# Performance work log

Hardware: AMD Instinct MI355X
Metric: run time of the kernel (lower is better)

Reference implementation:

```python
import jax, jax.numpy as jnp
import numpy as np

N_NODES = 50000
N_EDGES = 800000
NUM_FEATURES = 128
H1, H2, H3 = 256, 512, 256


def setup_inputs() -> dict:
    key = jax.random.key(0)
    ks = jax.random.split(key, 14)

    def lin(kw, fan_in, fan_out):
        # torch nn.Linear-style init, stored as [in, out] for x @ W
        bound = 1.0 / np.sqrt(fan_in)
        W = jax.random.uniform(kw, (fan_in, fan_out), jnp.float32, -bound, bound)
        b = jnp.zeros((fan_out,), jnp.float32)
        return W, b

    x = jax.random.normal(ks[0], (N_NODES, NUM_FEATURES), jnp.float32)
    edge_index = jax.random.randint(ks[1], (2, N_EDGES), 0, N_NODES, jnp.int64 if jax.config.jax_enable_x64 else jnp.int32)

    W1, b1 = lin(ks[2], NUM_FEATURES, H1)
    W2, b2 = lin(ks[3], H1, H2)
    W3, b3 = lin(ks[4], H2, H3)
    Wf1, bf1 = lin(ks[5], H3, 128)
    Wf2, bf2 = lin(ks[6], 128, 64)
    Wf3, bf3 = lin(ks[7], 64, 1)

    return {"x": x, "edge_index": edge_index,
            "W1": W1, "b1": b1, "W2": W2, "b2": b2, "W3": W3, "b3": b3,
            "Wf1": Wf1, "bf1": bf1, "Wf2": Wf2, "bf2": bf2, "Wf3": Wf3, "bf3": bf3}


def gcn_conv(x, W, b, row, col, dinv_row_col, n):
    # PyG GCNConv: out = D^{-1/2} (A+I) D^{-1/2} (x W) + b, self-loops already in row/col
    h = x @ W                              # [N, out]
    msg = h[row] * dinv_row_col[:, None]   # gather + edge-wise scale: [E+N, out]
    return jax.ops.segment_sum(msg, col, num_segments=n) + b


def reference(x, edge_index, W1, b1, W2, b2, W3, b3, Wf1, bf1, Wf2, bf2, Wf3, bf3):
    n = x.shape[0]
    loop = jnp.arange(n, dtype=edge_index.dtype)
    row = jnp.concatenate([edge_index[0], loop])   # sources (with self-loops)
    col = jnp.concatenate([edge_index[1], loop])   # targets (with self-loops)

    # symmetric normalization (computed once; identical for all three convs)
    deg = jax.ops.segment_sum(jnp.ones(col.shape[0], x.dtype), col, num_segments=n)
    dinv = jnp.where(deg > 0, jax.lax.rsqrt(deg), 0.0)
    norm = dinv[row] * dinv[col]                   # [E+N]

    h = jax.nn.relu(gcn_conv(x, W1, b1, row, col, norm, n))
    h = jax.nn.relu(gcn_conv(h, W2, b2, row, col, norm, n))
    h = jax.nn.relu(gcn_conv(h, W3, b3, row, col, norm, n))

    g = jnp.mean(h, axis=0, keepdims=True)         # [1, H3]
    g = jax.nn.relu(g @ Wf1 + bf1)
    g = jax.nn.relu(g @ Wf2 + bf2)
    return g @ Wf3 + bf3                           # [1, 1]
```

## Files before the change

kernel.cpp:

```cpp
#include <hip/hip_runtime.h>
#include <hip/hip_bf16.h>

#define N_NODES 50000
#define N_EDGES 800000
#define N_BUCKETS 64
#define M_PAD 50048
#define SCAN_NB 196

typedef short short8 __attribute__((ext_vector_type(8)));
typedef float floatx4 __attribute__((ext_vector_type(4)));

__device__ __forceinline__ unsigned short f2bf(float f) {
    unsigned u = __float_as_uint(f);
    unsigned r = (u + 0x7fff + ((u >> 16) & 1)) >> 16;
    return (unsigned short)r;
}
__device__ __forceinline__ float bf2f(unsigned short h) {
    return __uint_as_float(((unsigned)h) << 16);
}
__device__ __forceinline__ void expand2(unsigned u, float& lo, float& hi) {
    lo = __uint_as_float(u << 16);
    hi = __uint_as_float(u & 0xffff0000u);
}
__device__ __forceinline__ void accum8(float* a, uint4 g, float w) {
    float lo, hi;
    expand2(g.x, lo, hi); a[0] += lo * w; a[1] += hi * w;
    expand2(g.y, lo, hi); a[2] += lo * w; a[3] += hi * w;
    expand2(g.z, lo, hi); a[4] += lo * w; a[5] += hi * w;
    expand2(g.w, lo, hi); a[6] += lo * w; a[7] += hi * w;
}

__device__ __forceinline__ void gload16(const void* gp, void* lp) {
    __builtin_amdgcn_global_load_lds(
        (const __attribute__((address_space(1))) unsigned int*)gp,
        (__attribute__((address_space(3))) unsigned int*)lp,
        16, 0, 0);
}

__global__ void k_init(int* __restrict__ cnt, float* __restrict__ gb) {
    int i = blockIdx.x * blockDim.x + threadIdx.x;
    if (i < N_NODES) cnt[i] = 0;
    if (i < N_BUCKETS * 256) gb[i] = 0.0f;
}

__global__ void k_count(const int* __restrict__ col, int* __restrict__ cnt) {
    int e = blockIdx.x * blockDim.x + threadIdx.x;
    if (e < N_EDGES) atomicAdd(&cnt[col[e]], 1);
}

__global__ __launch_bounds__(256) void k_scanA(const int* __restrict__ cnt,
                                               int* __restrict__ bsum) {
    __shared__ int red[256];
    int t = threadIdx.x;
    int i = blockIdx.x * 256 + t;
    red[t] = (i < N_NODES) ? cnt[i] : 0;
    __syncthreads();
    for (int d = 128; d > 0; d >>= 1) {
        if (t < d) red[t] += red[t + d];
        __syncthreads();
    }
    if (t == 0) bsum[blockIdx.x] = red[0];
}

__global__ __launch_bounds__(256) void k_scanB(const int* __restrict__ bsum,
                                               int* __restrict__ bbase,
                                               int* __restrict__ off) {
    __shared__ int sc[256];
    int t = threadIdx.x;
    sc[t] = (t < SCAN_NB) ? bsum[t] : 0;
    __syncthreads();
    for (int d = 1; d < 256; d <<= 1) {
        int v = 0;
        if (t >= d) v = sc[t - d];
        __syncthreads();
        if (t >= d) sc[t] += v;
        __syncthreads();
    }
    if (t < SCAN_NB) bbase[t] = sc[t] - bsum[t];
    if (t == 0) off[N_NODES] = N_EDGES + N_NODES;
    if (t == 0) off[N_NODES] = N_EDGES;
}

__global__ __launch_bounds__(256) void k_scanC(const int* __restrict__ cnt,
                                               const int* __restrict__ bbase,
                                               int* __restrict__ off,
                                               int* __restrict__ cursor,
                                               float* __restrict__ dinv) {
    __shared__ int sc[256];
    int t = threadIdx.x;
    int i = blockIdx.x * 256 + t;
    int c = (i < N_NODES) ? cnt[i] : 0;
    sc[t] = c;
    __syncthreads();
    for (int d = 1; d < 256; d <<= 1) {
        int v = 0;
        if (t >= d) v = sc[t - d];
        __syncthreads();
        if (t >= d) sc[t] += v;
        __syncthreads();
    }
    if (i < N_NODES) {
        int excl = sc[t] - c + bbase[blockIdx.x];
        off[i] = excl;
        cursor[i] = excl;
        dinv[i] = 1.0f / sqrtf((float)(c + 1));
    }
}

__global__ void k_fill(const int* __restrict__ row, const int* __restrict__ col,
                       const float* __restrict__ dinv, int* __restrict__ cursor,
                       int2* __restrict__ epack) {
    int e = blockIdx.x * blockDim.x + threadIdx.x;
    if (e >= N_EDGES) return;
    int v = col[e];
    int p = atomicAdd(&cursor[v], 1);
    int r = row[e];
    epack[p] = make_int2(r, __float_as_int(dinv[r]));
}

__global__ void k_prepW(const float* __restrict__ W,
                        unsigned short* __restrict__ Th,
                        unsigned short* __restrict__ Tl, int K, int N) {
    int idx = blockIdx.x * blockDim.x + threadIdx.x;
    if (idx >= K * N) return;
    int n = idx / K, k = idx - n * K;
    float v = W[(size_t)k * N + n];
    unsigned short h = f2bf(v);
    Th[idx] = h;
    Tl[idx] = f2bf(v - bf2f(h));
}

__global__ void k_prepX(const float* __restrict__ x, unsigned short* __restrict__ xb) {
    int i = blockIdx.x * blockDim.x + threadIdx.x;
    if (i < N_NODES * 128) xb[i] = f2bf(x[i]);
}

template <int DIM, int POOL>
__global__ __launch_bounds__(256) void k_aggb(
    const unsigned short* __restrict__ xb, const int* __restrict__ off,
    const int2* __restrict__ epack, const float* __restrict__ dinv,
    const float* __restrict__ bias, unsigned short* __restrict__ outb,
    float* __restrict__ gb) {
    const int LPN = DIM / 8;
    const int NPB = 256 / LPN;
    __shared__ float gpart[256];
    if (POOL) {
        gpart[threadIdx.x] = 0.0f;
        __syncthreads();
    }
    int v = blockIdx.x * NPB + threadIdx.x / LPN;
    int f = (threadIdx.x % LPN) * 8;
    float dv = dinv[v];
    const unsigned short* __restrict__ xf = xb + f;
    float a0[8], a1[8], a2[8], a3[8];
    {
        uint4 sv = *(const uint4*)&xf[(size_t)v * DIM];
        float e0, e1;
        expand2(sv.x, e0, e1); a0[0] = e0 * dv; a0[1] = e1 * dv;
        expand2(sv.y, e0, e1); a0[2] = e0 * dv; a0[3] = e1 * dv;
        expand2(sv.z, e0, e1); a0[4] = e0 * dv; a0[5] = e1 * dv;
        expand2(sv.w, e0, e1); a0[6] = e0 * dv; a0[7] = e1 * dv;
#pragma unroll
        for (int i = 0; i < 8; ++i) { a1[i] = 0.f; a2[i] = 0.f; a3[i] = 0.f; }
    }
    int s = off[v], e = off[v + 1];
    int j = s;
    for (; j + 4 <= e; j += 4) {
        int2 p0 = epack[j + 0];
        int2 p1 = epack[j + 1];
        int2 p2 = epack[j + 2];
        int2 p3 = epack[j + 3];
        uint4 g0 = *(const uint4*)&xf[(size_t)p0.x * DIM];
        uint4 g1 = *(const uint4*)&xf[(size_t)p1.x * DIM];
        uint4 g2 = *(const uint4*)&xf[(size_t)p2.x * DIM];
        uint4 g3 = *(const uint4*)&xf[(size_t)p3.x * DIM];
        accum8(a0, g0, __int_as_float(p0.y));
        accum8(a1, g1, __int_as_float(p1.y));
        accum8(a2, g2, __int_as_float(p2.y));
        accum8(a3, g3, __int_as_float(p3.y));
    }
    for (; j < e; ++j) {
        int2 p = epack[j];
        uint4 g = *(const uint4*)&xf[(size_t)p.x * DIM];
        accum8(a0, g, __int_as_float(p.y));
    }
    float acc[8];
#pragma unroll
    for (int i = 0; i < 8; ++i)
        acc[i] = ((a0[i] + a1[i]) + (a2[i] + a3[i])) * dv;
    if (!POOL) {
        uint4 o;
        o.x = (unsigned)f2bf(acc[0]) | ((unsigned)f2bf(acc[1]) << 16);
        o.y = (unsigned)f2bf(acc[2]) | ((unsigned)f2bf(acc[3]) << 16);
        o.z = (unsigned)f2bf(acc[4]) | ((unsigned)f2bf(acc[5]) << 16);
        o.w = (unsigned)f2bf(acc[6]) | ((unsigned)f2bf(acc[7]) << 16);
        *(uint4*)&outb[(size_t)v * DIM + f] = o;
    } else {
#pragma unroll
        for (int i = 0; i < 8; ++i) {
            float r = fmaxf(acc[i] + bias[f + i], 0.0f);
            atomicAdd(&gpart[f + i], r);
        }
        __syncthreads();
        atomicAdd(&gb[(blockIdx.x & (N_BUCKETS - 1)) * 256 + threadIdx.x],
                  gpart[threadIdx.x]);
    }
}

template <int BIAS, int RELU>
__global__ __launch_bounds__(256) void k_gemm_b(
    const unsigned short* __restrict__ A,
    const unsigned short* __restrict__ Bh, const unsigned short* __restrict__ Bl,
    const float* __restrict__ bias, unsigned short* __restrict__ C,
    int M, int K, int N) {
    __shared__ unsigned short As[2][128 * 32];
    __shared__ unsigned short BsH[2][128 * 32];
    __shared__ unsigned short BsL[2][128 * 32];
    int tid = threadIdx.x;
    int lane = tid & 63;
    int w = tid >> 6;
    int wr = w & 1, wc = w >> 1;
    int bm = blockIdx.x * 128, bn = blockIdx.y * 128;

    floatx4 acc[4][4];
    floatx4 zero = {0.f, 0.f, 0.f, 0.f};
#pragma unroll
    for (int t = 0; t < 4; ++t)
#pragma unroll
        for (int u = 0; u < 4; ++u) acc[t][u] = zero;

    int c0 = w * 2, c1 = c0 + 1;
    int srow = lane >> 2;
    int kg = ((lane & 3) - ((lane >> 3) & 3)) & 3;
    int kc = kg * 8;
    const unsigned short* Ap0 = A + (size_t)(bm + c0 * 16 + srow) * K + kc;
    const unsigned short* Ap1 = A + (size_t)(bm + c1 * 16 + srow) * K + kc;
    const unsigned short* Bh0 = Bh + (size_t)(bn + c0 * 16 + srow) * K + kc;
    const unsigned short* Bh1 = Bh + (size_t)(bn + c1 * 16 + srow) * K + kc;
    const unsigned short* Bl0 = Bl + (size_t)(bn + c0 * 16 + srow) * K + kc;
    const unsigned short* Bl1 = Bl + (size_t)(bn + c1 * 16 + srow) * K + kc;

    const int KT = K >> 5;
#define STAGE(half, k0)                                   \
    do {                                                  \
        gload16(Ap0 + (k0), &As[half][c0 * 512]);         \
        gload16(Ap1 + (k0), &As[half][c1 * 512]);         \
        gload16(Bh0 + (k0), &BsH[half][c0 * 512]);        \
        gload16(Bh1 + (k0), &BsH[half][c1 * 512]);        \
        gload16(Bl0 + (k0), &BsL[half][c0 * 512]);        \
        gload16(Bl1 + (k0), &BsL[half][c1 * 512]);        \
    } while (0)

    STAGE(0, 0);
    __syncthreads();

    int fr = lane & 15;
    int fq = lane >> 4;
    int cl = ((fq + (fr >> 1)) & 3) * 8;

    for (int kt = 0; kt < KT; ++kt) {
        int half = kt & 1;
        if (kt + 1 < KT) STAGE(1 - half, (kt + 1) * 32);
        short8 av[4], bhv[4], blv[4];
#pragma unroll
        for (int t = 0; t < 4; ++t) {
            av[t]  = *(const short8*)&As[half][(wr * 64 + t * 16 + fr) * 32 + cl];
            bhv[t] = *(const short8*)&BsH[half][(wc * 64 + t * 16 + fr) * 32 + cl];
            blv[t] = *(const short8*)&BsL[half][(wc * 64 + t * 16 + fr) * 32 + cl];
        }
#pragma unroll
        for (int t = 0; t < 4; ++t)
#pragma unroll
            for (int u = 0; u < 4; ++u) {
                acc[t][u] = __builtin_amdgcn_mfma_f32_16x16x32_bf16(av[t], bhv[u], acc[t][u], 0, 0, 0);
                acc[t][u] = __builtin_amdgcn_mfma_f32_16x16x32_bf16(av[t], blv[u], acc[t][u], 0, 0, 0);
            }
        __syncthreads();
    }
#undef STAGE

#pragma unroll
    for (int u = 0; u < 4; ++u) {
        int colg = bn + wc * 64 + u * 16 + fr;
        float bv = BIAS ? bias[colg] : 0.0f;
#pragma unroll
        for (int t = 0; t < 4; ++t) {
#pragma unroll
            for (int r = 0; r < 4; ++r) {
                int rowg = bm + wr * 64 + t * 16 + fq * 4 + r;
                if (rowg < M) {
                    float o = acc[t][u][r] + bv;
                    if (RELU) o = fmaxf(o, 0.f);
                    C[(size_t)rowg * N + colg] = f2bf(o);
                }
            }
        }
    }
}

__global__ void k_mlp(const float* __restrict__ gb,
                      const float* __restrict__ Wf1, const float* __restrict__ bf1,
                      const float* __restrict__ Wf2, const float* __restrict__ bf2,
                      const float* __restrict__ Wf3, const float* __restrict__ bf3,
                      float* __restrict__ out) {
    __shared__ float s0[256], s1[128], s2[64];
    int t = threadIdx.x;
    float sum = 0.0f;
    for (int b = 0; b < N_BUCKETS; ++b) sum += gb[b * 256 + t];
    s0[t] = sum * (1.0f / (float)N_NODES);
    __syncthreads();
    if (t < 128) {
        float a = bf1[t];
        for (int k = 0; k < 256; ++k) a += s0[k] * Wf1[k * 128 + t];
        s1[t] = fmaxf(a, 0.0f);
    }
    __syncthreads();
    if (t < 64) {
        float a = bf2[t];
        for (int k = 0; k < 128; ++k) a += s1[k] * Wf2[k * 64 + t];
        s2[t] = fmaxf(a, 0.0f);
    }
    __syncthreads();
    if (t == 0) {
        float a = bf3[0];
        for (int k = 0; k < 64; ++k) a += s2[k] * Wf3[k];
        out[0] = a;
    }
}

extern "C" void kernel_launch(void* const* d_in, const int* in_sizes, int n_in,
                              void* d_out, int out_size, void* d_ws, size_t ws_size,
                              hipStream_t stream) {
    const float* x  = (const float*)d_in[0];
    const int* ei   = (const int*)d_in[1];
    const float* W1 = (const float*)d_in[2];
    const float* b1 = (const float*)d_in[3];
    const float* W2 = (const float*)d_in[4];
    const float* b2 = (const float*)d_in[5];
    const float* W3 = (const float*)d_in[6];
    const float* b3 = (const float*)d_in[7];
    const float* Wf1 = (const float*)d_in[8];
    const float* bf1 = (const float*)d_in[9];
    const float* Wf2 = (const float*)d_in[10];
    const float* bf2 = (const float*)d_in[11];
    const float* Wf3 = (const float*)d_in[12];
    const float* bf3 = (const float*)d_in[13];
    float* out = (float*)d_out;

    char* p = (char*)d_ws;
    auto alloc = [&](size_t bytes) {
        void* r = (void*)p;
        p += (bytes + 255) & ~((size_t)255);
        return r;
    };
    int*   cnt    = (int*)  alloc(N_NODES * sizeof(int));
    int*   off    = (int*)  alloc((N_NODES + 1) * sizeof(int));
    int*   cursor = (int*)  alloc(N_NODES * sizeof(int));
    int*   bsum   = (int*)  alloc(SCAN_NB * sizeof(int));
    int*   bbase  = (int*)  alloc(SCAN_NB * sizeof(int));
    float* dinv   = (float*)alloc(N_NODES * sizeof(float));
    int2*  epack  = (int2*) alloc((size_t)N_EDGES * sizeof(int2));
    float* gb     = (float*)alloc(N_BUCKETS * 256 * sizeof(float));
    unsigned short* W1h = (unsigned short*)alloc(128 * 256 * 2);
    unsigned short* W1l = (unsigned short*)alloc(128 * 256 * 2);
    unsigned short* W2h = (unsigned short*)alloc(256 * 512 * 2);
    unsigned short* W2l = (unsigned short*)alloc(256 * 512 * 2);
    unsigned short* W3h = (unsigned short*)alloc(512 * 256 * 2);
    unsigned short* W3l = (unsigned short*)alloc(512 * 256 * 2);
    unsigned short* xb = (unsigned short*)alloc((size_t)N_NODES * 128 * 2);
    unsigned short* t0 = (unsigned short*)alloc((size_t)M_PAD * 128 * 2);
    unsigned short* h1 = (unsigned short*)alloc((size_t)N_NODES * 256 * 2);
    unsigned short* t1 = (unsigned short*)alloc((size_t)M_PAD * 256 * 2);
    unsigned short* h2 = (unsigned short*)alloc((size_t)M_PAD * 512 * 2);
    unsigned short* t2 = (unsigned short*)alloc((size_t)N_NODES * 256 * 2);

    const int* row = ei;
    const int* col = ei + N_EDGES;

    const int NB = (N_NODES + 255) / 256;
    const int EB = (N_EDGES + 255) / 256;

    k_init<<<NB, 256, 0, stream>>>(cnt, gb);
    k_count<<<EB, 256, 0, stream>>>(col, cnt);
    k_scanA<<<SCAN_NB, 256, 0, stream>>>(cnt, bsum);
    k_scanB<<<1, 256, 0, stream>>>(bsum, bbase, off);
    k_scanC<<<SCAN_NB, 256, 0, stream>>>(cnt, bbase, off, cursor, dinv);
    k_fill<<<EB, 256, 0, stream>>>(row, col, dinv, cursor, epack);

    k_prepW<<<(128 * 256 + 255) / 256, 256, 0, stream>>>(W1, W1h, W1l, 128, 256);
    k_prepW<<<(256 * 512 + 255) / 256, 256, 0, stream>>>(W2, W2h, W2l, 256, 512);
    k_prepW<<<(512 * 256 + 255) / 256, 256, 0, stream>>>(W3, W3h, W3l, 512, 256);
    k_prepX<<<(N_NODES * 128 + 255) / 256, 256, 0, stream>>>(x, xb);

    const int M = N_NODES;
    const int MB = (M + 127) / 128;

    k_aggb<128, 0><<<N_NODES / 16, 256, 0, stream>>>(
        xb, off, epack, dinv, nullptr, t0, nullptr);
    {
        dim3 grid(MB, 256 / 128);
        k_gemm_b<1, 1><<<grid, 256, 0, stream>>>(t0, W1h, W1l, b1, h1, M, 128, 256);
    }
    k_aggb<256, 0><<<N_NODES / 8, 256, 0, stream>>>(
        h1, off, epack, dinv, nullptr, t1, nullptr);
    {
        dim3 grid(MB, 512 / 128);
        k_gemm_b<1, 1><<<grid, 256, 0, stream>>>(t1, W2h, W2l, b2, h2, M, 256, 512);
    }
    {
        dim3 grid(MB, 256 / 128);
        k_gemm_b<0, 0><<<grid, 256, 0, stream>>>(h2, W3h, W3l, nullptr, t2, M, 512, 256);
    }
    k_aggb<256, 1><<<N_NODES / 8, 256, 0, stream>>>(
        t2, off, epack, dinv, b3, nullptr, gb);

    k_mlp<<<1, 256, 0, stream>>>(gb, Wf1, bf1, Wf2, bf2, Wf3, bf3, out);
}
```

Measured before the change: 532.7 us.

## Slice node features into column blocks so aggregation gathers fit in cache

Features are stored in a sliced layout of 8 column slices, each holding contiguous [N_NODES x DIM/8] rows. Each aggregation block handles one slice, so the random neighbour gathers touch a much smaller working set that can stay in L2/MALL. The GEMMs that feed the aggregations write directly in the sliced layout. In exchange the edge list is re-read 8 times, the GEMM stores become more scattered, and accumulation moves from four accumulators to one, with fewer lanes per node.

After: 546.3 us. 1.03x slower.

```diff
diff --git a/kernel.cpp b/kernel.cpp
--- a/kernel.cpp
+++ b/kernel.cpp
@@ -77,7 +77,6 @@
         __syncthreads();
     }
     if (t < SCAN_NB) bbase[t] = sc[t] - bsum[t];
-    if (t == 0) off[N_NODES] = N_EDGES + N_NODES;
     if (t == 0) off[N_NODES] = N_EDGES;
 }
 
@@ -130,76 +129,79 @@
     Tl[idx] = f2bf(v - bf2f(h));
 }
 
-__global__ void k_prepX(const float* __restrict__ x, unsigned short* __restrict__ xb) {
+__global__ void k_prepX(const float* __restrict__ x, unsigned short* __restrict__ xs) {
     int i = blockIdx.x * blockDim.x + threadIdx.x;
-    if (i < N_NODES * 128) xb[i] = f2bf(x[i]);
+    if (i >= N_NODES * 128) return;
+    int v = i >> 7, k = i & 127;
+    int sl = k >> 4, w = k & 15;
+    xs[(size_t)sl * N_NODES * 16 + (size_t)v * 16 + w] = f2bf(x[i]);
 }
 
 template <int DIM, int POOL>
-__global__ __launch_bounds__(256) void k_aggb(
-    const unsigned short* __restrict__ xb, const int* __restrict__ off,
+__global__ __launch_bounds__(256) void k_aggs(
+    const unsigned short* __restrict__ xs, const int* __restrict__ off,
     const int2* __restrict__ epack, const float* __restrict__ dinv,
     const float* __restrict__ bias, unsigned short* __restrict__ outb,
     float* __restrict__ gb) {
-    const int LPN = DIM / 8;
+    const int SW = DIM / 8;
+    const int LPN = SW / 8;
     const int NPB = 256 / LPN;
     __shared__ float gpart[256];
     if (POOL) {
         gpart[threadIdx.x] = 0.0f;
         __syncthreads();
     }
-    int v = blockIdx.x * NPB + threadIdx.x / LPN;
-    int f = (threadIdx.x % LPN) * 8;
-    float dv = dinv[v];
-    const unsigned short* __restrict__ xf = xb + f;
-    float a0[8], a1[8], a2[8], a3[8];
-    {
-        uint4 sv = *(const uint4*)&xf[(size_t)v * DIM];
-        float e0, e1;
-        expand2(sv.x, e0, e1); a0[0] = e0 * dv; a0[1] = e1 * dv;
-        expand2(sv.y, e0, e1); a0[2] = e0 * dv; a0[3] = e1 * dv;
-        expand2(sv.z, e0, e1); a0[4] = e0 * dv; a0[5] = e1 * dv;
-        expand2(sv.w, e0, e1); a0[6] = e0 * dv; a0[7] = e1 * dv;
-#pragma unroll
-        for (int i = 0; i < 8; ++i) { a1[i] = 0.f; a2[i] = 0.f; a3[i] = 0.f; }
-    }
-    int s = off[v], e = off[v + 1];
-    int j = s;
-    for (; j + 4 <= e; j += 4) {
-        int2 p0 = epack[j + 0];
-        int2 p1 = epack[j + 1];
-        int2 p2 = epack[j + 2];
-        int2 p3 = epack[j + 3];
-        uint4 g0 = *(const uint4*)&xf[(size_t)p0.x * DIM];
-        uint4 g1 = *(const uint4*)&xf[(size_t)p1.x * DIM];
-        uint4 g2 = *(const uint4*)&xf[(size_t)p2.x * DIM];
-        uint4 g3 = *(const uint4*)&xf[(size_t)p3.x * DIM];
-        accum8(a0, g0, __int_as_float(p0.y));
-        accum8(a1, g1, __int_as_float(p1.y));
-        accum8(a2, g2, __int_as_float(p2.y));
-        accum8(a3, g3, __int_as_float(p3.y));
-    }
-    for (; j < e; ++j) {
-        int2 p = epack[j];
-        uint4 g = *(const uint4*)&xf[(size_t)p.x * DIM];
-        accum8(a0, g, __int_as_float(p.y));
-    }
+    int sl = blockIdx.x & 7;
+    int chunk = blockIdx.x >> 3;
+    int v = chunk * NPB + threadIdx.x / LPN;
+    int li = threadIdx.x % LPN;
+    const unsigned short* __restrict__ xsl =
+        xs + (size_t)sl * N_NODES * SW + li * 8;
     float acc[8];
 #pragma unroll
-    for (int i = 0; i < 8; ++i)
-        acc[i] = ((a0[i] + a1[i]) + (a2[i] + a3[i])) * dv;
+    for (int i = 0; i < 8; ++i) acc[i] = 0.f;
+    float dv = 0.f;
+    if (v < N_NODES) {
+        dv = dinv[v];
+        uint4 sv = *(const uint4*)&xsl[(size_t)v * SW];
+        accum8(acc, sv, dv);
+        int s0 = off[v], e0 = off[v + 1];
+        int j = s0;
+        for (; j + 4 <= e0; j += 4) {
+            int2 p0 = epack[j + 0];
+            int2 p1 = epack[j + 1];
+            int2 p2 = epack[j + 2];
+            int2 p3 = epack[j + 3];
+            uint4 g0 = *(const uint4*)&xsl[(size_t)p0.x * SW];
+            uint4 g1 = *(const uint4*)&xsl[(size_t)p1.x * SW];
+            uint4 g2 = *(const uint4*)&xsl[(size_t)p2.x * SW];
+            uint4 g3 = *(const uint4*)&xsl[(size_t)p3.x * SW];
+            accum8(acc, g0, __int_as_float(p0.y));
+            accum8(acc, g1, __int_as_float(p1.y));
+            accum8(acc, g2, __int_as_float(p2.y));
+            accum8(acc, g3, __int_as_float(p3.y));
+        }
+        for (; j < e0; ++j) {
+            int2 p = epack[j];
+            uint4 g = *(const uint4*)&xsl[(size_t)p.x * SW];
+            accum8(acc, g, __int_as_float(p.y));
+        }
+    }
+    int fg = sl * SW + li * 8;
     if (!POOL) {
-        uint4 o;
-        o.x = (unsigned)f2bf(acc[0]) | ((unsigned)f2bf(acc[1]) << 16);
-        o.y = (unsigned)f2bf(acc[2]) | ((unsigned)f2bf(acc[3]) << 16);
-        o.z = (unsigned)f2bf(acc[4]) | ((unsigned)f2bf(acc[5]) << 16);
-        o.w = (unsigned)f2bf(acc[6]) | ((unsigned)f2bf(acc[7]) << 16);
-        *(uint4*)&outb[(size_t)v * DIM + f] = o;
+        if (v < N_NODES) {
+            uint4 o;
+            o.x = (unsigned)f2bf(acc[0] * dv) | ((unsigned)f2bf(acc[1] * dv) << 16);
+            o.y = (unsigned)f2bf(acc[2] * dv) | ((unsigned)f2bf(acc[3] * dv) << 16);
+            o.z = (unsigned)f2bf(acc[4] * dv) | ((unsigned)f2bf(acc[5] * dv) << 16);
+            o.w = (unsigned)f2bf(acc[6] * dv) | ((unsigned)f2bf(acc[7] * dv) << 16);
+            *(uint4*)&outb[(size_t)v * DIM + fg] = o;
+        }
     } else {
 #pragma unroll
         for (int i = 0; i < 8; ++i) {
-            float r = fmaxf(acc[i] + bias[f + i], 0.0f);
-            atomicAdd(&gpart[f + i], r);
+            float r = (v < N_NODES) ? fmaxf(acc[i] * dv + bias[fg + i], 0.f) : 0.f;
+            atomicAdd(&gpart[fg + i], r);
         }
         __syncthreads();
         atomicAdd(&gb[(blockIdx.x & (N_BUCKETS - 1)) * 256 + threadIdx.x],
@@ -207,7 +209,7 @@
     }
 }
 
-template <int BIAS, int RELU>
+template <int BIAS, int RELU, int SLICED>
 __global__ __launch_bounds__(256) void k_gemm_b(
     const unsigned short* __restrict__ A,
     const unsigned short* __restrict__ Bh, const unsigned short* __restrict__ Bl,
@@ -291,7 +293,12 @@
                 if (rowg < M) {
                     float o = acc[t][u][r] + bv;
                     if (RELU) o = fmaxf(o, 0.f);
-                    C[(size_t)rowg * N + colg] = f2bf(o);
+                    if (SLICED) {
+                        C[(size_t)(colg >> 5) * N_NODES * 32 +
+                          (size_t)rowg * 32 + (colg & 31)] = f2bf(o);
+                    } else {
+                        C[(size_t)rowg * N + colg] = f2bf(o);
+                    }
                 }
             }
         }
@@ -367,12 +374,12 @@
     unsigned short* W2l = (unsigned short*)alloc(256 * 512 * 2);
     unsigned short* W3h = (unsigned short*)alloc(512 * 256 * 2);
     unsigned short* W3l = (unsigned short*)alloc(512 * 256 * 2);
-    unsigned short* xb = (unsigned short*)alloc((size_t)N_NODES * 128 * 2);
-    unsigned short* t0 = (unsigned short*)alloc((size_t)M_PAD * 128 * 2);
-    unsigned short* h1 = (unsigned short*)alloc((size_t)N_NODES * 256 * 2);
-    unsigned short* t1 = (unsigned short*)alloc((size_t)M_PAD * 256 * 2);
-    unsigned short* h2 = (unsigned short*)alloc((size_t)M_PAD * 512 * 2);
-    unsigned short* t2 = (unsigned short*)alloc((size_t)N_NODES * 256 * 2);
+    unsigned short* xbs = (unsigned short*)alloc((size_t)N_NODES * 128 * 2);
+    unsigned short* t0  = (unsigned short*)alloc((size_t)M_PAD * 128 * 2);
+    unsigned short* h1s = (unsigned short*)alloc((size_t)N_NODES * 256 * 2);
+    unsigned short* t1  = (unsigned short*)alloc((size_t)M_PAD * 256 * 2);
+    unsigned short* h2  = (unsigned short*)alloc((size_t)M_PAD * 512 * 2);
+    unsigned short* t2s = (unsigned short*)alloc((size_t)N_NODES * 256 * 2);
 
     const int* row = ei;
     const int* col = ei + N_EDGES;
@@ -390,29 +397,29 @@
     k_prepW<<<(128 * 256 + 255) / 256, 256, 0, stream>>>(W1, W1h, W1l, 128, 256);
     k_prepW<<<(256 * 512 + 255) / 256, 256, 0, stream>>>(W2, W2h, W2l, 256, 512);
     k_prepW<<<(512 * 256 + 255) / 256, 256, 0, stream>>>(W3, W3h, W3l, 512, 256);
-    k_prepX<<<(N_NODES * 128 + 255) / 256, 256, 0, stream>>>(x, xb);
+    k_prepX<<<(N_NODES * 128 + 255) / 256, 256, 0, stream>>>(x, xbs);
 
     const int M = N_NODES;
     const int MB = (M + 127) / 128;
 
-    k_aggb<128, 0><<<N_NODES / 16, 256, 0, stream>>>(
-        xb, off, epack, dinv, nullptr, t0, nullptr);
+    k_aggs<128, 0><<<8 * ((N_NODES + 127) / 128), 256, 0, stream>>>(
+        xbs, off, epack, dinv, nullptr, t0, nullptr);
     {
         dim3 grid(MB, 256 / 128);
-        k_gemm_b<1, 1><<<grid, 256, 0, stream>>>(t0, W1h, W1l, b1, h1, M, 128, 256);
-    }
-    k_aggb<256, 0><<<N_NODES / 8, 256, 0, stream>>>(
-        h1, off, epack, dinv, nullptr, t1, nullptr);
+        k_gemm_b<1, 1, 1><<<grid, 256, 0, stream>>>(t0, W1h, W1l, b1, h1s, M, 128, 256);
+    }
+    k_aggs<256, 0><<<8 * ((N_NODES + 63) / 64), 256, 0, stream>>>(
+        h1s, off, epack, dinv, nullptr, t1, nullptr);
     {
         dim3 grid(MB, 512 / 128);
-        k_gemm_b<1, 1><<<grid, 256, 0, stream>>>(t1, W2h, W2l, b2, h2, M, 256, 512);
+        k_gemm_b<1, 1, 0><<<grid, 256, 0, stream>>>(t1, W2h, W2l, b2, h2, M, 256, 512);
     }
     {
         dim3 grid(MB, 256 / 128);
-        k_gemm_b<0, 0><<<grid, 256, 0, stream>>>(h2, W3h, W3l, nullptr, t2, M, 512, 256);
-    }
-    k_aggb<256, 1><<<N_NODES / 8, 256, 0, stream>>>(
-        t2, off, epack, dinv, b3, nullptr, gb);
+        k_gemm_b<0, 0, 1><<<grid, 256, 0, stream>>>(h2, W3h, W3l, nullptr, t2s, M, 512, 256);
+    }
+    k_aggs<256, 1><<<8 * ((N_NODES + 63) / 64), 256, 0, stream>>>(
+        t2s, off, epack, dinv, b3, nullptr, gb);
 
     k_mlp<<<1, 256, 0, stream>>>(gb, Wf1, bf1, Wf2, bf2, Wf3, bf3, out);
 }
```

## Assign one wavefront per node in aggregation, splitting edges across sub-groups

Applied to the files above, without the earlier changes.

The aggregation kernel now maps one 64-lane wavefront to each destination node. The lanes are split into sub-groups that each take different edges, and the partial sums are combined with cross-lane shuffles. The old scheme had a fixed group of lanes walk all of a node's edges serially. The new one raises memory-level parallelism per node and shortens the longest per-node loop, but lanes sit idle when a node has few edges and the grid has more blocks. A redundant store of the offset sentinel is also removed.

Result: no change. 529.2 us (-0.6%).

```diff
diff --git a/kernel.cpp b/kernel.cpp
--- a/kernel.cpp
+++ b/kernel.cpp
@@ -77,7 +77,6 @@
         __syncthreads();
     }
     if (t < SCAN_NB) bbase[t] = sc[t] - bsum[t];
-    if (t == 0) off[N_NODES] = N_EDGES + N_NODES;
     if (t == 0) off[N_NODES] = N_EDGES;
 }
 
@@ -136,70 +135,77 @@
 }
 
 template <int DIM, int POOL>
-__global__ __launch_bounds__(256) void k_aggb(
+__global__ __launch_bounds__(256) void k_aggw2(
     const unsigned short* __restrict__ xb, const int* __restrict__ off,
     const int2* __restrict__ epack, const float* __restrict__ dinv,
     const float* __restrict__ bias, unsigned short* __restrict__ outb,
     float* __restrict__ gb) {
-    const int LPN = DIM / 8;
-    const int NPB = 256 / LPN;
+    const int LPE = DIM / 8;
+    const int SEG = 64 / LPE;
     __shared__ float gpart[256];
     if (POOL) {
         gpart[threadIdx.x] = 0.0f;
         __syncthreads();
     }
-    int v = blockIdx.x * NPB + threadIdx.x / LPN;
-    int f = (threadIdx.x % LPN) * 8;
+    int wv = threadIdx.x >> 6;
+    int li = threadIdx.x & 63;
+    int v = blockIdx.x * 4 + wv;
+    int sub = li / LPE;
+    int fl = (li % LPE) * 8;
     float dv = dinv[v];
-    const unsigned short* __restrict__ xf = xb + f;
-    float a0[8], a1[8], a2[8], a3[8];
-    {
+    const unsigned short* __restrict__ xf = xb + fl;
+    float aA[8], aB[8];
+#pragma unroll
+    for (int i = 0; i < 8; ++i) { aA[i] = 0.f; aB[i] = 0.f; }
+    if (sub == 0) {
         uint4 sv = *(const uint4*)&xf[(size_t)v * DIM];
-        float e0, e1;
-        expand2(sv.x, e0, e1); a0[0] = e0 * dv; a0[1] = e1 * dv;
-        expand2(sv.y, e0, e1); a0[2] = e0 * dv; a0[3] = e1 * dv;
-        expand2(sv.z, e0, e1); a0[4] = e0 * dv; a0[5] = e1 * dv;
-        expand2(sv.w, e0, e1); a0[6] = e0 * dv; a0[7] = e1 * dv;
-#pragma unroll
-        for (int i = 0; i < 8; ++i) { a1[i] = 0.f; a2[i] = 0.f; a3[i] = 0.f; }
+        accum8(aA, sv, dv);
     }
     int s = off[v], e = off[v + 1];
     int j = s;
-    for (; j + 4 <= e; j += 4) {
-        int2 p0 = epack[j + 0];
-        int2 p1 = epack[j + 1];
-        int2 p2 = epack[j + 2];
-        int2 p3 = epack[j + 3];
+    for (; j + 2 * SEG <= e; j += 2 * SEG) {
+        int2 p0 = epack[j + sub];
+        int2 p1 = epack[j + SEG + sub];
         uint4 g0 = *(const uint4*)&xf[(size_t)p0.x * DIM];
         uint4 g1 = *(const uint4*)&xf[(size_t)p1.x * DIM];
-        uint4 g2 = *(const uint4*)&xf[(size_t)p2.x * DIM];
-        uint4 g3 = *(const uint4*)&xf[(size_t)p3.x * DIM];
-        accum8(a0, g0, __int_as_float(p0.y));
-        accum8(a1, g1, __int_as_float(p1.y));
-        accum8(a2, g2, __int_as_float(p2.y));
-        accum8(a3, g3, __int_as_float(p3.y));
-    }
-    for (; j < e; ++j) {
-        int2 p = epack[j];
-        uint4 g = *(const uint4*)&xf[(size_t)p.x * DIM];
-        accum8(a0, g, __int_as_float(p.y));
+        accum8(aA, g0, __int_as_float(p0.y));
+        accum8(aB, g1, __int_as_float(p1.y));
+    }
+    for (; j < e; j += SEG) {
+        int je = j + sub;
+        if (je < e) {
+            int2 p = epack[je];
+            uint4 g = *(const uint4*)&xf[(size_t)p.x * DIM];
+            accum8(aA, g, __int_as_float(p.y));
+        }
     }
     float acc[8];
 #pragma unroll
-    for (int i = 0; i < 8; ++i)
-        acc[i] = ((a0[i] + a1[i]) + (a2[i] + a3[i])) * dv;
+    for (int i = 0; i < 8; ++i) acc[i] = aA[i] + aB[i];
+    if (SEG >= 4) {
+#pragma unroll
+        for (int i = 0; i < 8; ++i) acc[i] += __shfl_xor(acc[i], 16, 64);
+    }
+#pragma unroll
+    for (int i = 0; i < 8; ++i) acc[i] += __shfl_xor(acc[i], 32, 64);
+#pragma unroll
+    for (int i = 0; i < 8; ++i) acc[i] *= dv;
     if (!POOL) {
-        uint4 o;
-        o.x = (unsigned)f2bf(acc[0]) | ((unsigned)f2bf(acc[1]) << 16);
-        o.y = (unsigned)f2bf(acc[2]) | ((unsigned)f2bf(acc[3]) << 16);
-        o.z = (unsigned)f2bf(acc[4]) | ((unsigned)f2bf(acc[5]) << 16);
-        o.w = (unsigned)f2bf(acc[6]) | ((unsigned)f2bf(acc[7]) << 16);
-        *(uint4*)&outb[(size_t)v * DIM + f] = o;
+        if (sub == 0) {
+            uint4 o;
+            o.x = (unsigned)f2bf(acc[0]) | ((unsigned)f2bf(acc[1]) << 16);
+            o.y = (unsigned)f2bf(acc[2]) | ((unsigned)f2bf(acc[3]) << 16);
+            o.z = (unsigned)f2bf(acc[4]) | ((unsigned)f2bf(acc[5]) << 16);
+            o.w = (unsigned)f2bf(acc[6]) | ((unsigned)f2bf(acc[7]) << 16);
+            *(uint4*)&outb[(size_t)v * DIM + fl] = o;
+        }
     } else {
-#pragma unroll
-        for (int i = 0; i < 8; ++i) {
-            float r = fmaxf(acc[i] + bias[f + i], 0.0f);
-            atomicAdd(&gpart[f + i], r);
+        if (sub == 0) {
+#pragma unroll
+            for (int i = 0; i < 8; ++i) {
+                float r = fmaxf(acc[i] + bias[fl + i], 0.0f);
+                atomicAdd(&gpart[fl + i], r);
+            }
         }
         __syncthreads();
         atomicAdd(&gb[(blockIdx.x & (N_BUCKETS - 1)) * 256 + threadIdx.x],
@@ -395,13 +401,13 @@
     const int M = N_NODES;
     const int MB = (M + 127) / 128;
 
-    k_aggb<128, 0><<<N_NODES / 16, 256, 0, stream>>>(
+    k_aggw2<128, 0><<<N_NODES / 4, 256, 0, stream>>>(
         xb, off, epack, dinv, nullptr, t0, nullptr);
     {
         dim3 grid(MB, 256 / 128);
         k_gemm_b<1, 1><<<grid, 256, 0, stream>>>(t0, W1h, W1l, b1, h1, M, 128, 256);
     }
-    k_aggb<256, 0><<<N_NODES / 8, 256, 0, stream>>>(
+    k_aggw2<256, 0><<<N_NODES / 4, 256, 0, stream>>>(
         h1, off, epack, dinv, nullptr, t1, nullptr);
     {
         dim3 grid(MB, 512 / 128);
@@ -411,7 +417,7 @@
         dim3 grid(MB, 256 / 128);
         k_gemm_b<0, 0><<<grid, 256, 0, stream>>>(h2, W3h, W3l, nullptr, t2, M, 512, 256);
     }
-    k_aggb<256, 1><<<N_NODES / 8, 256, 0, stream>>>(
+    k_aggw2<256, 1><<<N_NODES / 4, 256, 0, stream>>>(
         t2, off, epack, dinv, b3, nullptr, gb);
 
     k_mlp<<<1, 256, 0, stream>>>(gb, Wf1, bf1, Wf2, bf2, Wf3, bf3, out);
```
